# Kernel optimization log

Measured on AMD Instinct MI355X. Metric: run time of the kernel, lower is better.

The kernel has to match this reference:

```python
import jax, jax.numpy as jnp
import numpy as np


def setup_inputs() -> dict:
    key = jax.random.key(0)
    k1, k2 = jax.random.split(key)
    pred = jax.random.normal(k1, (4, 8192, 3), dtype=jnp.float32)
    target = jax.random.normal(k2, (4, 8192, 3), dtype=jnp.float32)
    return {"pred": pred, "target": target}


def reference(pred, target):
    # Squared pairwise distances: ||p||^2 + ||q||^2 - 2 p.q  -> (B, N1, N2)
    p2 = jnp.sum(pred * pred, axis=-1)          # (B, N1)
    q2 = jnp.sum(target * target, axis=-1)      # (B, N2)
    pq = jnp.einsum('bnd,bmd->bnm', pred, target)  # (B, N1, N2)
    d2 = jnp.maximum(p2[:, :, None] + q2[:, None, :] - 2.0 * pq, 0.0)
    forward_dist = jnp.min(d2, axis=2).mean(axis=1)   # (B,)
    backward_dist = jnp.min(d2, axis=1).mean(axis=1)  # (B,)
    chamfer = forward_dist + backward_dist
    return chamfer.mean()  # reduction='mean'
```

## Files before the change

### kernel.cpp

```cpp
#include <hip/hip_runtime.h>


#define NPTS   8192
#define BATCH  4
#define RPT    8
#define BLOCK  256
#define PTILE  (RPT * BLOCK)
#define NTILES (NPTS / PTILE)
#define CHUNK  128
#define NCHUNK (NPTS / CHUNK)
#define NMINS  (2 * BATCH * NPTS)

__global__ __launch_bounds__(BLOCK, 1) void chamfer_pairs(
    const float* __restrict__ pred, const float* __restrict__ target,
    int* __restrict__ mins)
{
    __shared__ float4 q4[CHUNK];
    __shared__ int    cmin_s[CHUNK];

    const int b = blockIdx.z;
    const float* __restrict__ P = pred   + b * NPTS * 3;
    const float* __restrict__ Q = target + b * NPTS * 3;

    const int tid = threadIdx.x;
    const int i0  = blockIdx.x * PTILE + tid;
    const int j0  = blockIdx.y * CHUNK;

    if (tid < CHUNK) {
        const float* qp = Q + 3 * (j0 + tid);
        const float qx = qp[0], qy = qp[1], qz = qp[2];
        q4[tid] = make_float4(qx, qy, qz, fmaf(qx, qx, fmaf(qy, qy, qz * qz)));
        cmin_s[tid] = 0x7F7F7F7F;
    }
    __syncthreads();

    float pxn[RPT], pyn[RPT], pzn[RPT], p2[RPT], m[RPT];
#pragma unroll
    for (int r = 0; r < RPT; ++r) {
        const float* pp = P + 3 * (i0 + r * BLOCK);
        const float x = pp[0], y = pp[1], z = pp[2];
        pxn[r] = -2.0f * x;
        pyn[r] = -2.0f * y;
        pzn[r] = -2.0f * z;
        p2[r]  = fmaf(x, x, fmaf(y, y, z * z));
        m[r]   = 3.0e38f;
    }

#pragma unroll 2
    for (int jj = 0; jj < CHUNK; ++jj) {
        const int j = (tid + jj) & (CHUNK - 1);
        const float4 q = q4[j];
        float d[RPT];
#pragma unroll
        for (int r = 0; r < RPT; ++r) {
            float t = fmaf(pxn[r], q.x, q.w);
            t = fmaf(pyn[r], q.y, t);
            t = fmaf(pzn[r], q.z, t);
            m[r] = fminf(m[r], t);
            d[r] = t + p2[r];
        }
        const float cm = fminf(fminf(fminf(d[0], d[1]), fminf(d[2], d[3])),
                               fminf(fminf(d[4], d[5]), fminf(d[6], d[7])));
        atomicMin(&cmin_s[j], __float_as_int(cm));
    }

    int* __restrict__ fwd = mins + b * NPTS;
    int* __restrict__ bwd = mins + (BATCH + b) * NPTS;
#pragma unroll
    for (int r = 0; r < RPT; ++r) {
        const float v = fmaxf(m[r] + p2[r], 0.0f);
        atomicMin(&fwd[i0 + r * BLOCK], __float_as_int(v));
    }
    __syncthreads();
    if (tid < CHUNK)
        atomicMin(&bwd[j0 + tid], cmin_s[tid]);
}

__global__ __launch_bounds__(256) void chamfer_reduce1(
    const int* __restrict__ mins, float* __restrict__ partials)
{
    __shared__ float part[4];
    const int base = blockIdx.x * 1024 + threadIdx.x;

    float s = fmaxf(__int_as_float(mins[base]),       0.0f) +
              fmaxf(__int_as_float(mins[base + 256]), 0.0f) +
              fmaxf(__int_as_float(mins[base + 512]), 0.0f) +
              fmaxf(__int_as_float(mins[base + 768]), 0.0f);

    for (int off = 32; off > 0; off >>= 1)
        s += __shfl_down(s, off, 64);
    if ((threadIdx.x & 63) == 0)
        part[threadIdx.x >> 6] = s;
    __syncthreads();

    if (threadIdx.x == 0)
        partials[blockIdx.x] = part[0] + part[1] + part[2] + part[3];
}

__global__ __launch_bounds__(64) void chamfer_reduce2(
    const float* __restrict__ partials, float* __restrict__ out)
{
    float t = partials[threadIdx.x];
    for (int off = 32; off > 0; off >>= 1)
        t += __shfl_down(t, off, 64);
    if (threadIdx.x == 0)
        out[0] = t * (1.0f / (float)(BATCH * NPTS));
}

extern "C" void kernel_launch(void* const* d_in, const int* in_sizes, int n_in,
                              void* d_out, int out_size, void* d_ws, size_t ws_size,
                              hipStream_t stream)
{
    const float* pred   = (const float*)d_in[0];
    const float* target = (const float*)d_in[1];
    float* out = (float*)d_out;
    int*   mins     = (int*)d_ws;
    float* partials = (float*)d_ws + NMINS;

    hipMemsetAsync(mins, 0x7F, (size_t)NMINS * sizeof(int), stream);

    dim3 grid(NTILES, NCHUNK, BATCH);
    chamfer_pairs<<<grid, BLOCK, 0, stream>>>(pred, target, mins);
    chamfer_reduce1<<<64, 256, 0, stream>>>(mins, partials);
    chamfer_reduce2<<<1, 64, 0, stream>>>(partials, out);
}
```

Baseline: 93.23 us.

## Use packed float2 FMA with SoA paired target layout in chamfer pair kernel

Moves the shared-memory target points from float4 AoS into four float2 SoA arrays, so each thread handles two target points per iteration with packed 2-wide FMAs (v_pk_fma_f32 on CDNA). The per-wave rotation offset is changed to stagger wavefronts across the pairs, and launch bounds now hint 4 blocks per CU instead of 1. The goal is to roughly halve the FMA instruction count in the inner loop. The cost is extra register pressure from the duplicated p-values and two LDS atomics per iteration.

After: 90.21 us. 3.2% less time.

```diff
diff --git a/kernel.cpp b/kernel.cpp
--- a/kernel.cpp
+++ b/kernel.cpp
@@ -1,5 +1,7 @@
 #include <hip/hip_runtime.h>
 
+
+typedef float f32x2 __attribute__((ext_vector_type(2)));
 
 #define NPTS   8192
 #define BATCH  4
@@ -8,15 +10,16 @@
 #define PTILE  (RPT * BLOCK)
 #define NTILES (NPTS / PTILE)
 #define CHUNK  128
+#define NPAIR  (CHUNK / 2)
 #define NCHUNK (NPTS / CHUNK)
 #define NMINS  (2 * BATCH * NPTS)
 
-__global__ __launch_bounds__(BLOCK, 1) void chamfer_pairs(
+__global__ __launch_bounds__(BLOCK, 4) void chamfer_pairs(
     const float* __restrict__ pred, const float* __restrict__ target,
     int* __restrict__ mins)
 {
-    __shared__ float4 q4[CHUNK];
-    __shared__ int    cmin_s[CHUNK];
+    __shared__ f32x2 qx2[NPAIR], qy2[NPAIR], qz2[NPAIR], qw2[NPAIR];
+    __shared__ int   cmin_s[CHUNK];
 
     const int b = blockIdx.z;
     const float* __restrict__ P = pred   + b * NPTS * 3;
@@ -29,46 +32,65 @@
     if (tid < CHUNK) {
         const float* qp = Q + 3 * (j0 + tid);
         const float qx = qp[0], qy = qp[1], qz = qp[2];
-        q4[tid] = make_float4(qx, qy, qz, fmaf(qx, qx, fmaf(qy, qy, qz * qz)));
+        ((float*)qx2)[tid] = qx;
+        ((float*)qy2)[tid] = qy;
+        ((float*)qz2)[tid] = qz;
+        ((float*)qw2)[tid] = fmaf(qx, qx, fmaf(qy, qy, qz * qz));
         cmin_s[tid] = 0x7F7F7F7F;
     }
     __syncthreads();
 
-    float pxn[RPT], pyn[RPT], pzn[RPT], p2[RPT], m[RPT];
+    f32x2 pxn2[RPT], pyn2[RPT], pzn2[RPT], p22[RPT];
+    float m[RPT];
 #pragma unroll
     for (int r = 0; r < RPT; ++r) {
         const float* pp = P + 3 * (i0 + r * BLOCK);
         const float x = pp[0], y = pp[1], z = pp[2];
-        pxn[r] = -2.0f * x;
-        pyn[r] = -2.0f * y;
-        pzn[r] = -2.0f * z;
-        p2[r]  = fmaf(x, x, fmaf(y, y, z * z));
-        m[r]   = 3.0e38f;
+        const float nx = -2.0f * x, ny = -2.0f * y, nz = -2.0f * z;
+        const float p2 = fmaf(x, x, fmaf(y, y, z * z));
+        pxn2[r] = (f32x2){nx, nx};
+        pyn2[r] = (f32x2){ny, ny};
+        pzn2[r] = (f32x2){nz, nz};
+        p22[r]  = (f32x2){p2, p2};
+        m[r]    = 3.0e38f;
     }
 
+    const int soff = (tid & 63) + ((tid >> 6) << 4);
+
 #pragma unroll 2
-    for (int jj = 0; jj < CHUNK; ++jj) {
-        const int j = (tid + jj) & (CHUNK - 1);
-        const float4 q = q4[j];
-        float d[RPT];
+    for (int jj = 0; jj < NPAIR; ++jj) {
+        const int jp = (soff + jj) & (NPAIR - 1);
+        const f32x2 qx = qx2[jp];
+        const f32x2 qy = qy2[jp];
+        const f32x2 qz = qz2[jp];
+        const f32x2 qw = qw2[jp];
+
+        f32x2 d[RPT];
 #pragma unroll
         for (int r = 0; r < RPT; ++r) {
-            float t = fmaf(pxn[r], q.x, q.w);
-            t = fmaf(pyn[r], q.y, t);
-            t = fmaf(pzn[r], q.z, t);
-            m[r] = fminf(m[r], t);
-            d[r] = t + p2[r];
+            f32x2 t = __builtin_elementwise_fma(pxn2[r], qx, qw);
+            t = __builtin_elementwise_fma(pyn2[r], qy, t);
+            t = __builtin_elementwise_fma(pzn2[r], qz, t);
+            m[r] = fminf(fminf(m[r], t.x), t.y);
+            d[r] = t + p22[r];
         }
-        const float cm = fminf(fminf(fminf(d[0], d[1]), fminf(d[2], d[3])),
-                               fminf(fminf(d[4], d[5]), fminf(d[6], d[7])));
-        atomicMin(&cmin_s[j], __float_as_int(cm));
+        const float cl = fminf(
+            fminf(fminf(fminf(d[0].x, d[1].x), d[2].x),
+                  fminf(fminf(d[3].x, d[4].x), d[5].x)),
+            fminf(d[6].x, d[7].x));
+        const float ch = fminf(
+            fminf(fminf(fminf(d[0].y, d[1].y), d[2].y),
+                  fminf(fminf(d[3].y, d[4].y), d[5].y)),
+            fminf(d[6].y, d[7].y));
+        atomicMin(&cmin_s[2 * jp],     __float_as_int(cl));
+        atomicMin(&cmin_s[2 * jp + 1], __float_as_int(ch));
     }
 
     int* __restrict__ fwd = mins + b * NPTS;
     int* __restrict__ bwd = mins + (BATCH + b) * NPTS;
 #pragma unroll
     for (int r = 0; r < RPT; ++r) {
-        const float v = fmaxf(m[r] + p2[r], 0.0f);
+        const float v = fmaxf(m[r] + p22[r].x, 0.0f);
         atomicMin(&fwd[i0 + r * BLOCK], __float_as_int(v));
     }
     __syncthreads();
```
